# Optimization experiments

Measured on AMD Instinct MI355X. Metric: run time of the kernel, lower is better.

## Reference

```python
import jax, jax.numpy as jnp
import numpy as np

N_NODES = 100000
BN_EPS = 1e-5


def setup_inputs() -> dict:
    key = jax.random.key(0)
    ks = jax.random.split(key, 20)
    d, h, h2, nc = 128, 128, 64, 10
    E = 1_600_000
    x = jax.random.normal(ks[0], (N_NODES, d), jnp.float32)
    ei = jax.random.randint(ks[1], (2, E), 0, N_NODES, jnp.int64)
    s = 0.05
    return {
        "x": x,
        "ei": ei,
        "W1l": jax.random.normal(ks[2], (d, h), jnp.float32) * s,
        "b1l": jax.random.normal(ks[3], (h,), jnp.float32) * s,
        "W1r": jax.random.normal(ks[4], (d, h), jnp.float32) * s,
        "g1": jax.random.uniform(ks[5], (h,), jnp.float32) + 0.5,
        "be1": jax.random.normal(ks[6], (h,), jnp.float32) * s,
        "m1": jax.random.normal(ks[7], (h,), jnp.float32) * s,
        "v1": jax.random.uniform(ks[8], (h,), jnp.float32) + 0.5,
        "W2l": jax.random.normal(ks[9], (h, h2), jnp.float32) * s,
        "b2l": jax.random.normal(ks[10], (h2,), jnp.float32) * s,
        "W2r": jax.random.normal(ks[11], (h, h2), jnp.float32) * s,
        "g2": jax.random.uniform(ks[12], (h2,), jnp.float32) + 0.5,
        "be2": jax.random.normal(ks[13], (h2,), jnp.float32) * s,
        "m2": jax.random.normal(ks[14], (h2,), jnp.float32) * s,
        "v2": jax.random.uniform(ks[15], (h2,), jnp.float32) + 0.5,
        "Wh": jax.random.normal(ks[16], (h2, nc), jnp.float32) * s,
        "bh": jax.random.normal(ks[17], (nc,), jnp.float32) * s,
    }


def _sage_conv(x, src, dst, Wl, bl, Wr):
    # PyG SAGEConv: out_i = lin_l(mean_{j->i} x_j) + lin_r(x_i)
    msg = x[src]                                              # [E, d] gather
    agg = jax.ops.segment_sum(msg, dst, num_segments=N_NODES)
    cnt = jax.ops.segment_sum(jnp.ones_like(dst, x.dtype), dst, num_segments=N_NODES)
    agg = agg / jnp.maximum(cnt, 1.0)[:, None]                # mean aggregation
    return agg @ Wl + bl + x @ Wr


def _bn(x, g, b, m, v):
    # eval-mode BatchNorm1d with running stats
    return (x - m) * (g * jax.lax.rsqrt(v + BN_EPS)) + b


def reference(x, ei, W1l, b1l, W1r, g1, be1, m1, v1,
              W2l, b2l, W2r, g2, be2, m2, v2, Wh, bh):
    src, dst = ei[0], ei[1]
    h = jax.nn.relu(_bn(_sage_conv(x, src, dst, W1l, b1l, W1r), g1, be1, m1, v1))
    # dropout p=0.1 inactive in eval mode
    h = jax.nn.relu(_bn(_sage_conv(h, src, dst, W2l, b2l, W2r), g2, be2, m2, v2))
    return h @ Wh + bh
```

## Files before the change

### kernel.cpp

```cpp
#include <hip/hip_runtime.h>
#include <hip/hip_bf16.h>
#include <stdint.h>

#define N_NODES 100000
constexpr float BN_EPS = 1e-5f;

typedef __bf16 bf16x8 __attribute__((ext_vector_type(8)));
typedef float f32x4 __attribute__((ext_vector_type(4)));

__global__ __launch_bounds__(256) void k_prep(const unsigned int* __restrict__ w, int E,
                                              int* __restrict__ idx32,
                                              int* __restrict__ rank,
                                              int* __restrict__ deg, int wpB,
                                              const float* __restrict__ W1l,
                                              const float* __restrict__ W1r,
                                              const float* __restrict__ W2l,
                                              const float* __restrict__ W2r,
                                              __bf16* __restrict__ Wt1hi,
                                              __bf16* __restrict__ Wt1lo,
                                              __bf16* __restrict__ Wt2hi,
                                              __bf16* __restrict__ Wt2lo) {
    if ((int)blockIdx.x < wpB) {
        int idx = blockIdx.x * 256 + threadIdx.x;
        const float* W; __bf16 *Whi, *Wlo; int halfN, lidx;
        if (idx < 2 * 128 * 128) {
            lidx = idx; halfN = 128; Whi = Wt1hi; Wlo = Wt1lo;
            W = ((lidx >> 7) < 128) ? W1l : W1r;
        } else {
            lidx = idx - 2 * 128 * 128;
            if (lidx >= 2 * 64 * 128) return;
            halfN = 64; Whi = Wt2hi; Wlo = Wt2lo;
            W = ((lidx >> 7) < 64) ? W2l : W2r;
        }
        int c = lidx >> 7, k = lidx & 127;
        int cc = (c < halfN) ? c : c - halfN;
        float v = W[(size_t)k * halfN + cc];
        __bf16 h = (__bf16)v;
        Whi[lidx] = h;
        Wlo[lidx] = (__bf16)(v - (float)h);
        return;
    }
    unsigned int wv = w[1 + 2 * (threadIdx.x & 63)];
    int f = __any(wv != 0);
    int e = (blockIdx.x - wpB) * 256 + threadIdx.x;
    if (e >= E) return;
    int s = (int)(f ? w[e] : w[2 * (size_t)e]);
    int d = (int)(f ? w[E + e] : w[2 * ((size_t)E + e)]);
    idx32[e] = s;
    idx32[E + e] = d;
    rank[e] = atomicAdd(&deg[d], 1);
}

__global__ __launch_bounds__(256) void k_scan1(const int* __restrict__ deg,
                                               int* __restrict__ offs,
                                               int* __restrict__ bsum, int n) {
    __shared__ int s[256];
    int t = threadIdx.x;
    int i = blockIdx.x * 256 + t;
    int v = (i < n) ? deg[i] : 0;
    s[t] = v;
    __syncthreads();
    for (int off = 1; off < 256; off <<= 1) {
        int add = (t >= off) ? s[t - off] : 0;
        __syncthreads();
        s[t] += add;
        __syncthreads();
    }
    if (i < n) offs[i] = s[t] - v;
    if (t == 255) bsum[blockIdx.x] = s[255];
}

__global__ __launch_bounds__(256) void k_scan2(int* __restrict__ bsum, int nb) {
    __shared__ int s[256];
    __shared__ int carry;
    int t = threadIdx.x;
    if (t == 0) carry = 0;
    __syncthreads();
    for (int base = 0; base < nb; base += 256) {
        int i = base + t;
        int v = (i < nb) ? bsum[i] : 0;
        s[t] = v;
        __syncthreads();
        for (int off = 1; off < 256; off <<= 1) {
            int add = (t >= off) ? s[t - off] : 0;
            __syncthreads();
            s[t] += add;
            __syncthreads();
        }
        if (i < nb) bsum[i] = s[t] - v + carry;
        __syncthreads();
        if (t == 0) carry += s[255];
        __syncthreads();
    }
}

__global__ void k_scan3(int* __restrict__ offs, const int* __restrict__ bsum,
                        int n, int E) {
    int i = blockIdx.x * blockDim.x + threadIdx.x;
    if (i < n) offs[i] += bsum[i >> 8];
    if (i == 0) offs[n] = E;
}

template <int SPLITC>
__device__ void mfma_body(const float* __restrict__ A,
                          const __bf16* __restrict__ Wthi,
                          const __bf16* __restrict__ Wtlo,
                          __bf16* __restrict__ Cl, float* __restrict__ Cr,
                          int M, int bid) {
    constexpr int K = 128;
    __shared__ __bf16 sB[2][128][40];
    const int tid = threadIdx.x;
    const int lane = tid & 63;
    const int wave = tid >> 6;
    const int row0 = bid * 128 + wave * 32;
    const int rlo = lane & 15;
    const int rhi = lane >> 4;

    const int sc = tid >> 1;
    const int sseg = (tid & 1) * 16;

    f32x4 acc[4][2][2] = {};

    for (int k0 = 0; k0 < K; k0 += 32) {
        if (k0) __syncthreads();
        {
            const __bf16* gh = Wthi + (size_t)sc * K + k0 + sseg;
            const __bf16* gl = Wtlo + (size_t)sc * K + k0 + sseg;
            *(bf16x8*)(&sB[0][sc][sseg])     = *(const bf16x8*)gh;
            *(bf16x8*)(&sB[0][sc][sseg + 8]) = *(const bf16x8*)(gh + 8);
            *(bf16x8*)(&sB[1][sc][sseg])     = *(const bf16x8*)gl;
            *(bf16x8*)(&sB[1][sc][sseg + 8]) = *(const bf16x8*)(gl + 8);
        }
        bf16x8 ahi[2], alo[2];
        #pragma unroll
        for (int wr = 0; wr < 2; ++wr) {
            int row = row0 + wr * 16 + rlo;
            row = row < M ? row : M - 1;
            const float* ap = A + (size_t)row * K + k0 + rhi * 8;
            float4 v0 = *(const float4*)ap;
            float4 v1 = *(const float4*)(ap + 4);
            float vv[8] = {v0.x, v0.y, v0.z, v0.w, v1.x, v1.y, v1.z, v1.w};
            #pragma unroll
            for (int i = 0; i < 8; ++i) {
                __bf16 h = (__bf16)vv[i];
                ahi[wr][i] = h;
                alo[wr][i] = (__bf16)(vv[i] - (float)h);
            }
        }
        __syncthreads();
        #pragma unroll
        for (int cs = 0; cs < 4; ++cs) {
            #pragma unroll
            for (int cf = 0; cf < 2; ++cf) {
                int c = cs * 32 + cf * 16 + rlo;
                bf16x8 bhi = *(const bf16x8*)(&sB[0][c][rhi * 8]);
                bf16x8 blo = *(const bf16x8*)(&sB[1][c][rhi * 8]);
                #pragma unroll
                for (int wr = 0; wr < 2; ++wr) {
                    f32x4 a = acc[cs][wr][cf];
                    a = __builtin_amdgcn_mfma_f32_16x16x32_bf16(ahi[wr], bhi, a, 0, 0, 0);
                    a = __builtin_amdgcn_mfma_f32_16x16x32_bf16(ahi[wr], blo, a, 0, 0, 0);
                    a = __builtin_amdgcn_mfma_f32_16x16x32_bf16(alo[wr], bhi, a, 0, 0, 0);
                    acc[cs][wr][cf] = a;
                }
            }
        }
    }

    #pragma unroll
    for (int cs = 0; cs < 4; ++cs)
        #pragma unroll
        for (int cf = 0; cf < 2; ++cf) {
            int c = cs * 32 + cf * 16 + rlo;
            #pragma unroll
            for (int wr = 0; wr < 2; ++wr)
                #pragma unroll
                for (int r = 0; r < 4; ++r) {
                    int row = row0 + wr * 16 + rhi * 4 + r;
                    if (row < M) {
                        float val = acc[cs][wr][cf][r];
                        if (c < SPLITC)
                            Cl[(size_t)row * SPLITC + c] = (__bf16)val;
                        else
                            Cr[(size_t)row * (128 - SPLITC) + (c - SPLITC)] = val;
                    }
                }
        }
}

__global__ __launch_bounds__(256) void k_mfma2(const float* __restrict__ A,
                                               const __bf16* __restrict__ Wthi,
                                               const __bf16* __restrict__ Wtlo,
                                               __bf16* __restrict__ Cl,
                                               float* __restrict__ Cr, int M) {
    mfma_body<64>(A, Wthi, Wtlo, Cl, Cr, M, blockIdx.x);
}

__global__ __launch_bounds__(256) void k_mfma_bin(const float* __restrict__ A,
                                                  const __bf16* __restrict__ Wthi,
                                                  const __bf16* __restrict__ Wtlo,
                                                  __bf16* __restrict__ Cl,
                                                  float* __restrict__ Cr, int M,
                                                  int G,
                                                  const int* __restrict__ idx32,
                                                  const int* __restrict__ rank,
                                                  const int* __restrict__ offs,
                                                  int* __restrict__ csr, int E) {
    int bid = blockIdx.x;
    if (bid < G) {
        mfma_body<128>(A, Wthi, Wtlo, Cl, nullptr, M, bid);
        return;
    }
    bid -= G;
    if (bid < G) {
        mfma_body<0>(A, Wthi + 128 * 128, Wtlo + 128 * 128, nullptr, Cr, M, bid);
        return;
    }
    bid -= G;
    int base = bid * 1024 + threadIdx.x;
    #pragma unroll
    for (int k = 0; k < 4; ++k) {
        int e = base + k * 256;
        if (e < E) {
            int d = idx32[E + e];
            csr[offs[d] + rank[e]] = idx32[e];
        }
    }
}

template <int LOGF>
__global__ __launch_bounds__(256) void k_agg(const __bf16* __restrict__ xl,
                                             const float* __restrict__ lin,
                                             const int* __restrict__ csr,
                                             const int* __restrict__ offs,
                                             const float* __restrict__ b,
                                             const float* __restrict__ g,
                                             const float* __restrict__ be,
                                             const float* __restrict__ m,
                                             const float* __restrict__ v,
                                             float* __restrict__ out, int N) {
    constexpr int F = 1 << LOGF;
    constexpr int NW = (F == 128) ? 8 : 4;
    int node = blockIdx.x * 4 + (threadIdx.x >> 6);
    if (node >= N) return;
    int lane = threadIdx.x & 63;
    int sub = lane >> 4;
    int col = lane & 15;
    int beg = offs[node], end = offs[node + 1];
    float inv = 1.0f / fmaxf((float)(end - beg), 1.0f);

    float sx[NW];
    #pragma unroll
    for (int j = 0; j < NW; ++j) sx[j] = 0.f;

    int e = beg;
    while (e < end) {
        int bl = min(64, end - e);
        int myidx = (lane < bl) ? csr[e + lane] : 0;
        int u = 0;
        for (; u + 8 <= bl; u += 8) {
            int s0 = __shfl(myidx, u + sub, 64);
            int s1 = __shfl(myidx, u + 4 + sub, 64);
            if constexpr (F == 128) {
                uint4 t0 = *(const uint4*)((const char*)xl + (size_t)s0 * 256 + col * 16);
                uint4 t1 = *(const uint4*)((const char*)xl + (size_t)s1 * 256 + col * 16);
                unsigned int w0[4] = {t0.x, t0.y, t0.z, t0.w};
                unsigned int w1[4] = {t1.x, t1.y, t1.z, t1.w};
                #pragma unroll
                for (int i = 0; i < 4; ++i) {
                    sx[2 * i]     += __uint_as_float(w0[i] << 16) + __uint_as_float(w1[i] << 16);
                    sx[2 * i + 1] += __uint_as_float(w0[i] & 0xffff0000u) + __uint_as_float(w1[i] & 0xffff0000u);
                }
            } else {
                uint2 t0 = *(const uint2*)((const char*)xl + (size_t)s0 * 128 + col * 8);
                uint2 t1 = *(const uint2*)((const char*)xl + (size_t)s1 * 128 + col * 8);
                unsigned int w0[2] = {t0.x, t0.y};
                unsigned int w1[2] = {t1.x, t1.y};
                #pragma unroll
                for (int i = 0; i < 2; ++i) {
                    sx[2 * i]     += __uint_as_float(w0[i] << 16) + __uint_as_float(w1[i] << 16);
                    sx[2 * i + 1] += __uint_as_float(w0[i] & 0xffff0000u) + __uint_as_float(w1[i] & 0xffff0000u);
                }
            }
        }
        for (; u + 4 <= bl; u += 4) {
            int s0 = __shfl(myidx, u + sub, 64);
            if constexpr (F == 128) {
                uint4 t0 = *(const uint4*)((const char*)xl + (size_t)s0 * 256 + col * 16);
                unsigned int w0[4] = {t0.x, t0.y, t0.z, t0.w};
                #pragma unroll
                for (int i = 0; i < 4; ++i) {
                    sx[2 * i]     += __uint_as_float(w0[i] << 16);
                    sx[2 * i + 1] += __uint_as_float(w0[i] & 0xffff0000u);
                }
            } else {
                uint2 t0 = *(const uint2*)((const char*)xl + (size_t)s0 * 128 + col * 8);
                unsigned int w0[2] = {t0.x, t0.y};
                #pragma unroll
                for (int i = 0; i < 2; ++i) {
                    sx[2 * i]     += __uint_as_float(w0[i] << 16);
                    sx[2 * i + 1] += __uint_as_float(w0[i] & 0xffff0000u);
                }
            }
        }
        if (u < bl) {
            int rr = u + sub;
            int s0 = __shfl(myidx, rr < bl ? rr : u, 64);
            bool ok = rr < bl;
            if constexpr (F == 128) {
                uint4 t0 = *(const uint4*)((const char*)xl + (size_t)s0 * 256 + col * 16);
                unsigned int w0[4] = {t0.x, t0.y, t0.z, t0.w};
                #pragma unroll
                for (int i = 0; i < 4; ++i) {
                    sx[2 * i]     += ok ? __uint_as_float(w0[i] << 16) : 0.f;
                    sx[2 * i + 1] += ok ? __uint_as_float(w0[i] & 0xffff0000u) : 0.f;
                }
            } else {
                uint2 t0 = *(const uint2*)((const char*)xl + (size_t)s0 * 128 + col * 8);
                unsigned int w0[2] = {t0.x, t0.y};
                #pragma unroll
                for (int i = 0; i < 2; ++i) {
                    sx[2 * i]     += ok ? __uint_as_float(w0[i] << 16) : 0.f;
                    sx[2 * i + 1] += ok ? __uint_as_float(w0[i] & 0xffff0000u) : 0.f;
                }
            }
        }
        e += bl;
    }

    #pragma unroll
    for (int j = 0; j < NW; ++j) {
        sx[j] += __shfl_xor(sx[j], 16, 64);
        sx[j] += __shfl_xor(sx[j], 32, 64);
    }

    if (sub == 0) {
        #pragma unroll
        for (int j = 0; j < NW; ++j) {
            int f = col * NW + j;
            size_t o = (size_t)node * F + f;
            float y = ((sx[j] * inv + b[f] + lin[o]) - m[f]) *
                      (g[f] * rsqrtf(v[f] + BN_EPS)) + be[f];
            out[o] = fmaxf(y, 0.f);
        }
    }
}

__global__ __launch_bounds__(256) void k_head(const float* __restrict__ h2,
                                              const float* __restrict__ Wh,
                                              const float* __restrict__ bh,
                                              float* __restrict__ out, int M) {
    __shared__ float sW[64 * 10];
    __shared__ float sb[10];
    for (int i = threadIdx.x; i < 640; i += 256) sW[i] = Wh[i];
    if (threadIdx.x < 10) sb[threadIdx.x] = bh[threadIdx.x];
    __syncthreads();
    int n = blockIdx.x * blockDim.x + threadIdx.x;
    if (n >= M) return;
    float acc[10];
    #pragma unroll
    for (int c = 0; c < 10; ++c) acc[c] = sb[c];
    const float* hr = h2 + (size_t)n * 64;
    #pragma unroll
    for (int k = 0; k < 64; ++k) {
        float hv = hr[k];
        #pragma unroll
        for (int c = 0; c < 10; ++c) acc[c] = fmaf(hv, sW[k * 10 + c], acc[c]);
    }
    #pragma unroll
    for (int c = 0; c < 10; ++c) out[(size_t)n * 10 + c] = acc[c];
}

static inline size_t align256(size_t x) { return (x + 255) & ~(size_t)255; }

extern "C" void kernel_launch(void* const* d_in, const int* in_sizes, int n_in,
                              void* d_out, int out_size, void* d_ws, size_t ws_size,
                              hipStream_t stream) {
    const float* x   = (const float*)d_in[0];
    const void*  ei  = d_in[1];
    const float* W1l = (const float*)d_in[2];
    const float* b1l = (const float*)d_in[3];
    const float* W1r = (const float*)d_in[4];
    const float* g1  = (const float*)d_in[5];
    const float* be1 = (const float*)d_in[6];
    const float* m1  = (const float*)d_in[7];
    const float* v1  = (const float*)d_in[8];
    const float* W2l = (const float*)d_in[9];
    const float* b2l = (const float*)d_in[10];
    const float* W2r = (const float*)d_in[11];
    const float* g2  = (const float*)d_in[12];
    const float* be2 = (const float*)d_in[13];
    const float* m2  = (const float*)d_in[14];
    const float* v2  = (const float*)d_in[15];
    const float* Wh  = (const float*)d_in[16];
    const float* bh  = (const float*)d_in[17];
    float* out = (float*)d_out;

    const int N = N_NODES;
    const int E = in_sizes[1] / 2;
    const int NB = (N + 255) / 256;

    char* p = (char*)d_ws;
    int* idx32 = (int*)p;  p += align256((size_t)2 * E * 4);
    int* rank  = (int*)p;  p += align256((size_t)E * 4);
    int* csr   = (int*)p;  p += align256((size_t)E * 4);
    int* offs  = (int*)p;  p += align256((size_t)(N + 1) * 4);
    int* deg   = (int*)p;  p += align256((size_t)N * 4);
    int* bsum  = (int*)p;  p += 4096;
    __bf16* Wt1hi = (__bf16*)p; p += align256((size_t)256 * 128 * 2);
    __bf16* Wt1lo = (__bf16*)p; p += align256((size_t)256 * 128 * 2);
    __bf16* Wt2hi = (__bf16*)p; p += align256((size_t)128 * 128 * 2);
    __bf16* Wt2lo = (__bf16*)p; p += align256((size_t)128 * 128 * 2);
    __bf16* xl = (__bf16*)p; p += align256((size_t)N * 128 * 2);
    float* xr  = (float*)p;  p += (size_t)N * 128 * 4;
    float* h   = (float*)p;  p += (size_t)N * 128 * 4;
    __bf16* t2l = xl;
    float* t2r  = xr;
    float* h2   = h;

    dim3 blk(256);

    const int WPB = (2 * 128 * 128 + 2 * 64 * 128 + 255) / 256;
    int prepB = (E + 255) / 256;
    hipMemsetAsync(deg, 0, (size_t)N * 4, stream);
    k_prep<<<dim3(WPB + prepB), blk, 0, stream>>>(
        (const unsigned int*)ei, E, idx32, rank, deg, WPB,
        W1l, W1r, W2l, W2r, Wt1hi, Wt1lo, Wt2hi, Wt2lo);

    k_scan1<<<dim3(NB), blk, 0, stream>>>(deg, offs, bsum, N);
    k_scan2<<<dim3(1), blk, 0, stream>>>(bsum, NB);
    k_scan3<<<dim3(NB), blk, 0, stream>>>(offs, bsum, N, E);

    int G = (N + 127) / 128;
    int binBlocks = (E + 1023) / 1024;
    k_mfma_bin<<<dim3(2 * G + binBlocks), blk, 0, stream>>>(
        x, Wt1hi, Wt1lo, xl, xr, N, G, idx32, rank, offs, csr, E);

    k_agg<7><<<dim3((N + 3) / 4), blk, 0, stream>>>(
        xl, xr, csr, offs, b1l, g1, be1, m1, v1, h, N);

    k_mfma2<<<dim3(G), blk, 0, stream>>>(h, Wt2hi, Wt2lo, t2l, t2r, N);
    k_agg<6><<<dim3((N + 3) / 4), blk, 0, stream>>>(
        t2l, t2r, csr, offs, b2l, g2, be2, m2, v2, h2, N);

    k_head<<<dim3((N + 255) / 256), blk, 0, stream>>>(h2, Wh, bh, out, N);
}
```

Measured before the change: 304.1 us.

## Store layer-1 hidden activations as bf16 and fold BatchNorm into precomputed scale/shift

After: 288.8 us. -5.0%, faster.

```diff
diff --git a/kernel.cpp b/kernel.cpp
--- a/kernel.cpp
+++ b/kernel.cpp
@@ -7,6 +7,12 @@
 
 typedef __bf16 bf16x8 __attribute__((ext_vector_type(8)));
 typedef float f32x4 __attribute__((ext_vector_type(4)));
+
+__device__ inline unsigned int pk2(float a, float b) {
+    __bf16 x = (__bf16)a, y = (__bf16)b;
+    return (unsigned int)__builtin_bit_cast(unsigned short, x) |
+           ((unsigned int)__builtin_bit_cast(unsigned short, y) << 16);
+}
 
 __global__ __launch_bounds__(256) void k_prep(const unsigned int* __restrict__ w, int E,
                                               int* __restrict__ idx32,
@@ -19,7 +25,18 @@
                                               __bf16* __restrict__ Wt1hi,
                                               __bf16* __restrict__ Wt1lo,
                                               __bf16* __restrict__ Wt2hi,
-                                              __bf16* __restrict__ Wt2lo) {
+                                              __bf16* __restrict__ Wt2lo,
+                                              const float* __restrict__ b1l,
+                                              const float* __restrict__ g1,
+                                              const float* __restrict__ be1,
+                                              const float* __restrict__ m1,
+                                              const float* __restrict__ v1,
+                                              const float* __restrict__ b2l,
+                                              const float* __restrict__ g2,
+                                              const float* __restrict__ be2,
+                                              const float* __restrict__ m2,
+                                              const float* __restrict__ v2,
+                                              float* __restrict__ bn) {
     if ((int)blockIdx.x < wpB) {
         int idx = blockIdx.x * 256 + threadIdx.x;
         const float* W; __bf16 *Whi, *Wlo; int halfN, lidx;
@@ -40,9 +57,23 @@
         Wlo[lidx] = (__bf16)(v - (float)h);
         return;
     }
+    if ((int)blockIdx.x == wpB) {
+        int t = threadIdx.x;
+        if (t < 128) {
+            float S = g1[t] * rsqrtf(v1[t] + BN_EPS);
+            bn[t] = S;
+            bn[128 + t] = (b1l[t] - m1[t]) * S + be1[t];
+        } else if (t < 192) {
+            int f = t - 128;
+            float S = g2[f] * rsqrtf(v2[f] + BN_EPS);
+            bn[256 + f] = S;
+            bn[320 + f] = (b2l[f] - m2[f]) * S + be2[f];
+        }
+        return;
+    }
     unsigned int wv = w[1 + 2 * (threadIdx.x & 63)];
     int f = __any(wv != 0);
-    int e = (blockIdx.x - wpB) * 256 + threadIdx.x;
+    int e = (blockIdx.x - wpB - 1) * 256 + threadIdx.x;
     if (e >= E) return;
     int s = (int)(f ? w[e] : w[2 * (size_t)e]);
     int d = (int)(f ? w[E + e] : w[2 * ((size_t)E + e)]);
@@ -188,12 +219,80 @@
         }
 }
 
-__global__ __launch_bounds__(256) void k_mfma2(const float* __restrict__ A,
+__global__ __launch_bounds__(256) void k_mfma2(const __bf16* __restrict__ A,
                                                const __bf16* __restrict__ Wthi,
                                                const __bf16* __restrict__ Wtlo,
                                                __bf16* __restrict__ Cl,
                                                float* __restrict__ Cr, int M) {
-    mfma_body<64>(A, Wthi, Wtlo, Cl, Cr, M, blockIdx.x);
+    constexpr int K = 128;
+    constexpr int SPLITC = 64;
+    __shared__ __bf16 sB[2][128][40];
+    const int tid = threadIdx.x;
+    const int lane = tid & 63;
+    const int wave = tid >> 6;
+    const int row0 = blockIdx.x * 128 + wave * 32;
+    const int rlo = lane & 15;
+    const int rhi = lane >> 4;
+    const int sc = tid >> 1;
+    const int sseg = (tid & 1) * 16;
+
+    f32x4 acc[4][2][2] = {};
+
+    for (int k0 = 0; k0 < K; k0 += 32) {
+        if (k0) __syncthreads();
+        {
+            const __bf16* gh = Wthi + (size_t)sc * K + k0 + sseg;
+            const __bf16* gl = Wtlo + (size_t)sc * K + k0 + sseg;
+            *(bf16x8*)(&sB[0][sc][sseg])     = *(const bf16x8*)gh;
+            *(bf16x8*)(&sB[0][sc][sseg + 8]) = *(const bf16x8*)(gh + 8);
+            *(bf16x8*)(&sB[1][sc][sseg])     = *(const bf16x8*)gl;
+            *(bf16x8*)(&sB[1][sc][sseg + 8]) = *(const bf16x8*)(gl + 8);
+        }
+        bf16x8 a[2];
+        #pragma unroll
+        for (int wr = 0; wr < 2; ++wr) {
+            int row = row0 + wr * 16 + rlo;
+            row = row < M ? row : M - 1;
+            a[wr] = *(const bf16x8*)(A + (size_t)row * K + k0 + rhi * 8);
+        }
+        __syncthreads();
+        #pragma unroll
+        for (int cs = 0; cs < 4; ++cs) {
+            #pragma unroll
+            for (int cf = 0; cf < 2; ++cf) {
+                int c = cs * 32 + cf * 16 + rlo;
+                bf16x8 bhi = *(const bf16x8*)(&sB[0][c][rhi * 8]);
+                bf16x8 blo = *(const bf16x8*)(&sB[1][c][rhi * 8]);
+                #pragma unroll
+                for (int wr = 0; wr < 2; ++wr) {
+                    f32x4 v = acc[cs][wr][cf];
+                    v = __builtin_amdgcn_mfma_f32_16x16x32_bf16(a[wr], bhi, v, 0, 0, 0);
+                    v = __builtin_amdgcn_mfma_f32_16x16x32_bf16(a[wr], blo, v, 0, 0, 0);
+                    acc[cs][wr][cf] = v;
+                }
+            }
+        }
+    }
+
+    #pragma unroll
+    for (int cs = 0; cs < 4; ++cs)
+        #pragma unroll
+        for (int cf = 0; cf < 2; ++cf) {
+            int c = cs * 32 + cf * 16 + rlo;
+            #pragma unroll
+            for (int wr = 0; wr < 2; ++wr)
+                #pragma unroll
+                for (int r = 0; r < 4; ++r) {
+                    int row = row0 + wr * 16 + rhi * 4 + r;
+                    if (row < M) {
+                        float val = acc[cs][wr][cf][r];
+                        if (c < SPLITC)
+                            Cl[(size_t)row * SPLITC + c] = (__bf16)val;
+                        else
+                            Cr[(size_t)row * (128 - SPLITC) + (c - SPLITC)] = val;
+                    }
+                }
+        }
 }
 
 __global__ __launch_bounds__(256) void k_mfma_bin(const float* __restrict__ A,
@@ -233,12 +332,9 @@
                                              const float* __restrict__ lin,
                                              const int* __restrict__ csr,
                                              const int* __restrict__ offs,
-                                             const float* __restrict__ b,
-                                             const float* __restrict__ g,
-                                             const float* __restrict__ be,
-                                             const float* __restrict__ m,
-                                             const float* __restrict__ v,
-                                             float* __restrict__ out, int N) {
+                                             const float* __restrict__ S,
+                                             const float* __restrict__ T,
+                                             void* __restrict__ out, int N) {
     constexpr int F = 1 << LOGF;
     constexpr int NW = (F == 128) ? 8 : 4;
     int node = blockIdx.x * 4 + (threadIdx.x >> 6);
@@ -335,13 +431,33 @@
     }
 
     if (sub == 0) {
-        #pragma unroll
-        for (int j = 0; j < NW; ++j) {
-            int f = col * NW + j;
-            size_t o = (size_t)node * F + f;
-            float y = ((sx[j] * inv + b[f] + lin[o]) - m[f]) *
-                      (g[f] * rsqrtf(v[f] + BN_EPS)) + be[f];
-            out[o] = fmaxf(y, 0.f);
+        if constexpr (F == 128) {
+            const float4* lp = (const float4*)(lin + (size_t)node * 128 + col * 8);
+            float4 l0 = lp[0], l1 = lp[1];
+            const float4* Sp = (const float4*)(S + col * 8);
+            const float4* Tp = (const float4*)(T + col * 8);
+            float4 Sa = Sp[0], Sb = Sp[1], Ta = Tp[0], Tb = Tp[1];
+            float lv[8] = {l0.x, l0.y, l0.z, l0.w, l1.x, l1.y, l1.z, l1.w};
+            float Sv[8] = {Sa.x, Sa.y, Sa.z, Sa.w, Sb.x, Sb.y, Sb.z, Sb.w};
+            float Tv[8] = {Ta.x, Ta.y, Ta.z, Ta.w, Tb.x, Tb.y, Tb.z, Tb.w};
+            unsigned int u[4];
+            #pragma unroll
+            for (int i = 0; i < 4; ++i) {
+                float y0 = fmaxf(fmaf(fmaf(sx[2 * i], inv, lv[2 * i]), Sv[2 * i], Tv[2 * i]), 0.f);
+                float y1 = fmaxf(fmaf(fmaf(sx[2 * i + 1], inv, lv[2 * i + 1]), Sv[2 * i + 1], Tv[2 * i + 1]), 0.f);
+                u[i] = pk2(y0, y1);
+            }
+            *(uint4*)((char*)out + (size_t)node * 256 + col * 16) = make_uint4(u[0], u[1], u[2], u[3]);
+        } else {
+            float4 l = *(const float4*)(lin + (size_t)node * 64 + col * 4);
+            float4 Sv = *(const float4*)(S + col * 4);
+            float4 Tv = *(const float4*)(T + col * 4);
+            float4 o;
+            o.x = fmaxf(fmaf(fmaf(sx[0], inv, l.x), Sv.x, Tv.x), 0.f);
+            o.y = fmaxf(fmaf(fmaf(sx[1], inv, l.y), Sv.y, Tv.y), 0.f);
+            o.z = fmaxf(fmaf(fmaf(sx[2], inv, l.z), Sv.z, Tv.z), 0.f);
+            o.w = fmaxf(fmaf(fmaf(sx[3], inv, l.w), Sv.w, Tv.w), 0.f);
+            *(float4*)((float*)out + (size_t)node * 64 + col * 4) = o;
         }
     }
 }
@@ -407,25 +523,27 @@
     int* offs  = (int*)p;  p += align256((size_t)(N + 1) * 4);
     int* deg   = (int*)p;  p += align256((size_t)N * 4);
     int* bsum  = (int*)p;  p += 4096;
+    float* bn  = (float*)p; p += 4096;
     __bf16* Wt1hi = (__bf16*)p; p += align256((size_t)256 * 128 * 2);
     __bf16* Wt1lo = (__bf16*)p; p += align256((size_t)256 * 128 * 2);
     __bf16* Wt2hi = (__bf16*)p; p += align256((size_t)128 * 128 * 2);
     __bf16* Wt2lo = (__bf16*)p; p += align256((size_t)128 * 128 * 2);
     __bf16* xl = (__bf16*)p; p += align256((size_t)N * 128 * 2);
     float* xr  = (float*)p;  p += (size_t)N * 128 * 4;
-    float* h   = (float*)p;  p += (size_t)N * 128 * 4;
+    __bf16* hb = (__bf16*)p; p += align256((size_t)N * 128 * 2);
     __bf16* t2l = xl;
     float* t2r  = xr;
-    float* h2   = h;
+    float* h2   = (float*)hb;
 
     dim3 blk(256);
 
     const int WPB = (2 * 128 * 128 + 2 * 64 * 128 + 255) / 256;
     int prepB = (E + 255) / 256;
     hipMemsetAsync(deg, 0, (size_t)N * 4, stream);
-    k_prep<<<dim3(WPB + prepB), blk, 0, stream>>>(
+    k_prep<<<dim3(WPB + 1 + prepB), blk, 0, stream>>>(
         (const unsigned int*)ei, E, idx32, rank, deg, WPB,
-        W1l, W1r, W2l, W2r, Wt1hi, Wt1lo, Wt2hi, Wt2lo);
+        W1l, W1r, W2l, W2r, Wt1hi, Wt1lo, Wt2hi, Wt2lo,
+        b1l, g1, be1, m1, v1, b2l, g2, be2, m2, v2, bn);
 
     k_scan1<<<dim3(NB), blk, 0, stream>>>(deg, offs, bsum, N);
     k_scan2<<<dim3(1), blk, 0, stream>>>(bsum, NB);
@@ -437,11 +555,11 @@
         x, Wt1hi, Wt1lo, xl, xr, N, G, idx32, rank, offs, csr, E);
 
     k_agg<7><<<dim3((N + 3) / 4), blk, 0, stream>>>(
-        xl, xr, csr, offs, b1l, g1, be1, m1, v1, h, N);
-
-    k_mfma2<<<dim3(G), blk, 0, stream>>>(h, Wt2hi, Wt2lo, t2l, t2r, N);
+        xl, xr, csr, offs, bn, bn + 128, hb, N);
+
+    k_mfma2<<<dim3(G), blk, 0, stream>>>(hb, Wt2hi, Wt2lo, t2l, t2r, N);
     k_agg<6><<<dim3((N + 3) / 4), blk, 0, stream>>>(
-        t2l, t2r, csr, offs, b2l, g2, be2, m2, v2, h2, N);
+        t2l, t2r, csr, offs, bn + 256, bn + 320, h2, N);
 
     k_head<<<dim3((N + 255) / 256), blk, 0, stream>>>(h2, Wh, bh, out, N);
 }
```
